# Performance work log

Measured on AMD Instinct MI355X. Metric: run time of the kernel, lower is better.

Reference implementation:

```python
import jax, jax.numpy as jnp
import numpy as np

GRID_SIDES = (16, 32, 64)  # levels=3, base_grid_size=16, expansion=2.0, grid_dimensions=2
BATCH, INPUT_DIM = 8192, 256


def setup_inputs() -> dict:
    key = jax.random.key(0)
    k0, k1, k2, k3 = jax.random.split(key, 4)
    x = jax.random.normal(k0, (BATCH, INPUT_DIM), dtype=jnp.float32)
    w1 = jax.random.normal(k1, (GRID_SIDES[0] ** 2, INPUT_DIM), dtype=jnp.float32)
    w2 = jax.random.normal(k2, (GRID_SIDES[1] ** 2, INPUT_DIM), dtype=jnp.float32)
    w3 = jax.random.normal(k3, (GRID_SIDES[2] ** 2, INPUT_DIM), dtype=jnp.float32)
    return {"x": x, "w1": w1, "w2": w2, "w3": w3}


def _som_level(x, w, side):
    # Squared Euclidean distances (B, N) via the expanded form; N = side*side.
    d2 = (
        jnp.sum(x * x, axis=1, keepdims=True)
        - 2.0 * (x @ w.T)
        + jnp.sum(w * w, axis=1)
    )
    bmu_flat = jnp.argmin(d2, axis=1)  # (B,)
    coords = jnp.stack(jnp.unravel_index(bmu_flat, (side, side)), axis=-1)  # (B, 2)
    # Quantization error = exact Euclidean distance to the BMU prototype.
    diff = x - w[bmu_flat]  # (B, D)
    q_err = jnp.sqrt(jnp.sum(diff * diff, axis=1))  # (B,)
    return coords, q_err


def reference(x, w1, w2, w3):
    c1, q1 = _som_level(x, w1, GRID_SIDES[0])
    c2, q2 = _som_level(x, w2, GRID_SIDES[1])
    c3, q3 = _som_level(x, w3, GRID_SIDES[2])
    return (c1, c2, c3, q1, q2, q3)
```

## Files before the change

### kernel.cpp

```cpp
#include <hip/hip_runtime.h>
#include <hip/hip_fp16.h>
#include <stdint.h>

#define DIM 256
#define KE  768
#define NW  5376

typedef _Float16 half8 __attribute__((ext_vector_type(8)));
typedef float floatx4 __attribute__((ext_vector_type(4)));

#define WS_WE_OFF    12582912
#define WS_WNORM_OFF 20840448
#define WS_XNORM_OFF 20861952
#define WS_BEST_OFF  20894720

__global__ __launch_bounds__(256) void conv_kernel(
    const float* __restrict__ x, const float* __restrict__ w1,
    const float* __restrict__ w2, const float* __restrict__ w3,
    ushort* __restrict__ Xe, ushort* __restrict__ We,
    float* __restrict__ wnorm, float* __restrict__ xnorm,
    unsigned long long* __restrict__ best) {
  if (blockIdx.x < 96) best[blockIdx.x * 256 + threadIdx.x] = ~0ull;
  int task = blockIdx.x * 4 + (threadIdx.x >> 6);
  int lane = threadIdx.x & 63;
  const float* src; ushort* dst; float* ndst; int isx;
  if (task < 8192) {
    src = x + (size_t)task * DIM; dst = Xe + (size_t)task * KE;
    ndst = xnorm + task; isx = 1;
  } else {
    int wi = task - 8192;
    if (wi < 256)       src = w1 + (size_t)wi * DIM;
    else if (wi < 1280) src = w2 + (size_t)(wi - 256) * DIM;
    else                src = w3 + (size_t)(wi - 1280) * DIM;
    dst = We + (size_t)wi * KE; ndst = wnorm + wi; isx = 0;
  }
  float4 v = *(const float4*)(src + lane * 4);
  float fv[4] = {v.x, v.y, v.z, v.w};
  float s = fv[0]*fv[0] + fv[1]*fv[1] + fv[2]*fv[2] + fv[3]*fv[3];
  #pragma unroll
  for (int o = 32; o > 0; o >>= 1) s += __shfl_xor(s, o);
  if (lane == 0) *ndst = s;

  ushort h[4], l[4];
  #pragma unroll
  for (int e = 0; e < 4; ++e) {
    __half hh = __float2half(fv[e]);
    float hf = __half2float(hh);
    __half ll = __float2half((fv[e] - hf) * 2048.0f);
    h[e] = __half_as_ushort(hh);
    l[e] = __half_as_ushort(ll);
  }
  ushort4 h4 = make_ushort4(h[0], h[1], h[2], h[3]);
  ushort4 l4 = make_ushort4(l[0], l[1], l[2], l[3]);
  if (isx) {
    *(ushort4*)(dst + lane * 4)        = h4;
    *(ushort4*)(dst + 256 + lane * 4)  = h4;
    *(ushort4*)(dst + 512 + lane * 4)  = l4;
  } else {
    *(ushort4*)(dst + lane * 4)        = h4;
    *(ushort4*)(dst + 256 + lane * 4)  = l4;
    *(ushort4*)(dst + 512 + lane * 4)  = h4;
  }
}

__global__ __launch_bounds__(256) void gemm_kernel(
    const ushort* __restrict__ Xe, const ushort* __restrict__ We,
    const float* __restrict__ xnorm, const float* __restrict__ wnorm,
    unsigned long long* __restrict__ best) {
  __shared__ __align__(16) ushort As[128 * 64];
  __shared__ __align__(16) ushort Bs[128 * 64];
  unsigned long long (*red)[128] = (unsigned long long (*)[128])As;

  const int cb = blockIdx.x;
  const int r0 = blockIdx.y * 128;
  const int n0 = cb * 128;
  int level, lbase;
  if (cb < 2)       { level = 0; lbase = 0; }
  else if (cb < 10) { level = 1; lbase = 256; }
  else              { level = 2; lbase = 1280; }

  const int t = threadIdx.x;
  const int w = t >> 6;
  const int lane = t & 63;
  const int ln = lane & 15, q = lane >> 4;
  const int wm = (w >> 1) * 64, wn = (w & 1) * 64;

  floatx4 acc[4][4];
  #pragma unroll
  for (int i = 0; i < 4; ++i)
    #pragma unroll
    for (int j = 0; j < 4; ++j) acc[i][j] = (floatx4)0.0f;

  for (int k0 = 0; k0 < KE; k0 += 64) {
    if (k0 == 256) {
      #pragma unroll
      for (int i = 0; i < 4; ++i)
        #pragma unroll
        for (int j = 0; j < 4; ++j) acc[i][j] *= 2048.0f;
    }
    #pragma unroll
    for (int it = 0; it < 4; ++it) {
      int p = it * 256 + t;
      int m = p >> 3;
      int c = (p & 7) ^ (m & 7);
      const ushort* ga = Xe + (size_t)(r0 + m) * KE + k0 + c * 8;
      const ushort* gb = We + (size_t)(n0 + m) * KE + k0 + c * 8;
      int lbase_chunks = it * 256 + (t & 192);
      __builtin_amdgcn_global_load_lds(
          (const __attribute__((address_space(1))) void*)ga,
          (__attribute__((address_space(3))) void*)(As + lbase_chunks * 8), 16, 0, 0);
      __builtin_amdgcn_global_load_lds(
          (const __attribute__((address_space(1))) void*)gb,
          (__attribute__((address_space(3))) void*)(Bs + lbase_chunks * 8), 16, 0, 0);
    }
    __syncthreads();
    #pragma unroll
    for (int s = 0; s < 2; ++s) {
      half8 a[4], b[4];
      #pragma unroll
      for (int mt = 0; mt < 4; ++mt) {
        int m = wm + mt * 16 + ln;
        int pos = m * 8 + ((s * 4 + q) ^ (m & 7));
        a[mt] = *(const half8*)&As[pos * 8];
      }
      #pragma unroll
      for (int nt = 0; nt < 4; ++nt) {
        int n = wn + nt * 16 + ln;
        int pos = n * 8 + ((s * 4 + q) ^ (n & 7));
        b[nt] = *(const half8*)&Bs[pos * 8];
      }
      #pragma unroll
      for (int mt = 0; mt < 4; ++mt)
        #pragma unroll
        for (int nt = 0; nt < 4; ++nt)
          acc[mt][nt] = __builtin_amdgcn_mfma_f32_16x16x32_f16(
              a[mt], b[nt], acc[mt][nt], 0, 0, 0);
    }
    __syncthreads();
  }

  float wnv[4];
  #pragma unroll
  for (int nt = 0; nt < 4; ++nt) wnv[nt] = wnorm[n0 + wn + nt * 16 + ln];

  #pragma unroll
  for (int mt = 0; mt < 4; ++mt) {
    #pragma unroll
    for (int r = 0; r < 4; ++r) {
      int rowl = wm + mt * 16 + q * 4 + r;
      float xnv = xnorm[r0 + rowl];
      unsigned long long bp = ~0ull;
      #pragma unroll
      for (int nt = 0; nt < 4; ++nt) {
        float d2 = fmaxf(xnv + wnv[nt] - acc[mt][nt][r] * 0.0009765625f, 0.0f);
        unsigned col = (unsigned)(n0 + wn + nt * 16 + ln - lbase);
        unsigned long long p =
            ((unsigned long long)__float_as_uint(d2) << 32) | col;
        bp = (p < bp) ? p : bp;
      }
      #pragma unroll
      for (int off = 1; off < 16; off <<= 1) {
        unsigned long long o = __shfl_xor(bp, off);
        bp = (o < bp) ? o : bp;
      }
      if (ln == 0) red[w & 1][rowl] = bp;
    }
  }
  __syncthreads();
  if (t < 128) {
    unsigned long long a = red[0][t], b = red[1][t];
    unsigned long long m = (a < b) ? a : b;
    atomicMin(&best[level * 8192 + r0 + t], m);
  }
}

__global__ __launch_bounds__(256) void finalize_kernel(
    const float* __restrict__ x, const float* __restrict__ w1,
    const float* __restrict__ w2, const float* __restrict__ w3,
    const unsigned long long* __restrict__ best, float* __restrict__ out) {
  int task = blockIdx.x * 4 + (threadIdx.x >> 6);
  int lane = threadIdx.x & 63;
  int level = task >> 13;
  int row = task & 8191;
  const float* w; unsigned side;
  if (level == 0)      { w = w1; side = 16; }
  else if (level == 1) { w = w2; side = 32; }
  else                 { w = w3; side = 64; }
  unsigned idx = (unsigned)(best[level * 8192 + row] & 0xFFFFFFFFull);
  float4 xv = *(const float4*)(x + (size_t)row * DIM + lane * 4);
  float4 wv = *(const float4*)(w + (size_t)idx * DIM + lane * 4);
  float dx = xv.x - wv.x, dy = xv.y - wv.y, dz = xv.z - wv.z, dw = xv.w - wv.w;
  float s = dx * dx + dy * dy + dz * dz + dw * dw;
  #pragma unroll
  for (int o = 32; o > 0; o >>= 1) s += __shfl_xor(s, o);
  if (lane == 0) {
    out[level * 16384 + row * 2 + 0] = (float)(idx / side);
    out[level * 16384 + row * 2 + 1] = (float)(idx % side);
    out[49152 + level * 8192 + row] = sqrtf(s);
  }
}

extern "C" void kernel_launch(void* const* d_in, const int* in_sizes, int n_in,
                              void* d_out, int out_size, void* d_ws, size_t ws_size,
                              hipStream_t stream) {
  const float* x  = (const float*)d_in[0];
  const float* w1 = (const float*)d_in[1];
  const float* w2 = (const float*)d_in[2];
  const float* w3 = (const float*)d_in[3];
  ushort* Xe = (ushort*)d_ws;
  ushort* We = (ushort*)((char*)d_ws + WS_WE_OFF);
  float* wnorm = (float*)((char*)d_ws + WS_WNORM_OFF);
  float* xnorm = (float*)((char*)d_ws + WS_XNORM_OFF);
  unsigned long long* best = (unsigned long long*)((char*)d_ws + WS_BEST_OFF);

  conv_kernel<<<3392, 256, 0, stream>>>(x, w1, w2, w3, Xe, We, wnorm, xnorm,
                                        best);
  gemm_kernel<<<dim3(42, 64), 256, 0, stream>>>(Xe, We, xnorm, wnorm, best);
  finalize_kernel<<<6144, 256, 0, stream>>>(x, w1, w2, w3, best, (float*)d_out);
}
```

Baseline: 162.8 us.

## Fuse conv, GEMM and finalize into one persistent kernel with grid barriers

Replaces the three kernel launches with a single persistent kernel of 896 blocks. Work items are grid-strided, and the phases are separated by software grid barriers built on an atomic counter that is reset by a memset. The aim is to remove launch gaps and tail effects between the phases. In exchange it adds barrier spin cost and a memset, relies on all blocks being co-resident (launch_bounds 256,5), and caps spinning with a timeout that could let a phase start early.

New measurement: 565.9 us. 248% more time.

```diff
diff --git a/kernel.cpp b/kernel.cpp
--- a/kernel.cpp
+++ b/kernel.cpp
@@ -4,7 +4,7 @@
 
 #define DIM 256
 #define KE  768
-#define NW  5376
+#define NBLK 896
 
 typedef _Float16 half8 __attribute__((ext_vector_type(8)));
 typedef float floatx4 __attribute__((ext_vector_type(4)));
@@ -13,190 +13,207 @@
 #define WS_WNORM_OFF 20840448
 #define WS_XNORM_OFF 20861952
 #define WS_BEST_OFF  20894720
-
-__global__ __launch_bounds__(256) void conv_kernel(
+#define WS_CTRL_OFF  21091328
+
+__device__ __forceinline__ void grid_barrier(unsigned* cnt, unsigned target) {
+  __syncthreads();
+  if (threadIdx.x == 0) {
+    __threadfence();
+    atomicAdd(cnt, 1u);
+    unsigned spins = 0;
+    while (atomicAdd(cnt, 0u) < target && spins < 4000000u) {
+      __builtin_amdgcn_s_sleep(2);
+      ++spins;
+    }
+    __threadfence();
+  }
+  __syncthreads();
+}
+
+__global__ __launch_bounds__(256, 5) void fused_kernel(
     const float* __restrict__ x, const float* __restrict__ w1,
     const float* __restrict__ w2, const float* __restrict__ w3,
     ushort* __restrict__ Xe, ushort* __restrict__ We,
     float* __restrict__ wnorm, float* __restrict__ xnorm,
-    unsigned long long* __restrict__ best) {
-  if (blockIdx.x < 96) best[blockIdx.x * 256 + threadIdx.x] = ~0ull;
-  int task = blockIdx.x * 4 + (threadIdx.x >> 6);
-  int lane = threadIdx.x & 63;
-  const float* src; ushort* dst; float* ndst; int isx;
-  if (task < 8192) {
-    src = x + (size_t)task * DIM; dst = Xe + (size_t)task * KE;
-    ndst = xnorm + task; isx = 1;
-  } else {
-    int wi = task - 8192;
-    if (wi < 256)       src = w1 + (size_t)wi * DIM;
-    else if (wi < 1280) src = w2 + (size_t)(wi - 256) * DIM;
-    else                src = w3 + (size_t)(wi - 1280) * DIM;
-    dst = We + (size_t)wi * KE; ndst = wnorm + wi; isx = 0;
-  }
-  float4 v = *(const float4*)(src + lane * 4);
-  float fv[4] = {v.x, v.y, v.z, v.w};
-  float s = fv[0]*fv[0] + fv[1]*fv[1] + fv[2]*fv[2] + fv[3]*fv[3];
-  #pragma unroll
-  for (int o = 32; o > 0; o >>= 1) s += __shfl_xor(s, o);
-  if (lane == 0) *ndst = s;
-
-  ushort h[4], l[4];
-  #pragma unroll
-  for (int e = 0; e < 4; ++e) {
-    __half hh = __float2half(fv[e]);
-    float hf = __half2float(hh);
-    __half ll = __float2half((fv[e] - hf) * 2048.0f);
-    h[e] = __half_as_ushort(hh);
-    l[e] = __half_as_ushort(ll);
-  }
-  ushort4 h4 = make_ushort4(h[0], h[1], h[2], h[3]);
-  ushort4 l4 = make_ushort4(l[0], l[1], l[2], l[3]);
-  if (isx) {
-    *(ushort4*)(dst + lane * 4)        = h4;
-    *(ushort4*)(dst + 256 + lane * 4)  = h4;
-    *(ushort4*)(dst + 512 + lane * 4)  = l4;
-  } else {
-    *(ushort4*)(dst + lane * 4)        = h4;
-    *(ushort4*)(dst + 256 + lane * 4)  = l4;
-    *(ushort4*)(dst + 512 + lane * 4)  = h4;
-  }
-}
-
-__global__ __launch_bounds__(256) void gemm_kernel(
-    const ushort* __restrict__ Xe, const ushort* __restrict__ We,
-    const float* __restrict__ xnorm, const float* __restrict__ wnorm,
-    unsigned long long* __restrict__ best) {
+    unsigned long long* __restrict__ best, unsigned* __restrict__ ctrl,
+    float* __restrict__ out) {
   __shared__ __align__(16) ushort As[128 * 64];
   __shared__ __align__(16) ushort Bs[128 * 64];
   unsigned long long (*red)[128] = (unsigned long long (*)[128])As;
 
-  const int cb = blockIdx.x;
-  const int r0 = blockIdx.y * 128;
-  const int n0 = cb * 128;
-  int level, lbase;
-  if (cb < 2)       { level = 0; lbase = 0; }
-  else if (cb < 10) { level = 1; lbase = 256; }
-  else              { level = 2; lbase = 1280; }
-
   const int t = threadIdx.x;
-  const int w = t >> 6;
+  const int wv = t >> 6;
   const int lane = t & 63;
+
+  if (blockIdx.x < 96) best[blockIdx.x * 256 + t] = ~0ull;
+  for (int task = blockIdx.x * 4 + wv; task < 13568; task += NBLK * 4) {
+    const float* src; ushort* dst; float* ndst; int isx;
+    if (task < 8192) {
+      src = x + (size_t)task * DIM; dst = Xe + (size_t)task * KE;
+      ndst = xnorm + task; isx = 1;
+    } else {
+      int wi = task - 8192;
+      if (wi < 256)       src = w1 + (size_t)wi * DIM;
+      else if (wi < 1280) src = w2 + (size_t)(wi - 256) * DIM;
+      else                src = w3 + (size_t)(wi - 1280) * DIM;
+      dst = We + (size_t)wi * KE; ndst = wnorm + wi; isx = 0;
+    }
+    float4 v = *(const float4*)(src + lane * 4);
+    float fv[4] = {v.x, v.y, v.z, v.w};
+    float s = fv[0]*fv[0] + fv[1]*fv[1] + fv[2]*fv[2] + fv[3]*fv[3];
+    #pragma unroll
+    for (int o = 32; o > 0; o >>= 1) s += __shfl_xor(s, o);
+    if (lane == 0) *ndst = s;
+
+    ushort h[4], l[4];
+    #pragma unroll
+    for (int e = 0; e < 4; ++e) {
+      __half hh = __float2half(fv[e]);
+      float hf = __half2float(hh);
+      __half ll = __float2half((fv[e] - hf) * 2048.0f);
+      h[e] = __half_as_ushort(hh);
+      l[e] = __half_as_ushort(ll);
+    }
+    ushort4 h4 = make_ushort4(h[0], h[1], h[2], h[3]);
+    ushort4 l4 = make_ushort4(l[0], l[1], l[2], l[3]);
+    if (isx) {
+      *(ushort4*)(dst + lane * 4)        = h4;
+      *(ushort4*)(dst + 256 + lane * 4)  = h4;
+      *(ushort4*)(dst + 512 + lane * 4)  = l4;
+    } else {
+      *(ushort4*)(dst + lane * 4)        = h4;
+      *(ushort4*)(dst + 256 + lane * 4)  = l4;
+      *(ushort4*)(dst + 512 + lane * 4)  = h4;
+    }
+  }
+  grid_barrier(ctrl, NBLK);
+
   const int ln = lane & 15, q = lane >> 4;
-  const int wm = (w >> 1) * 64, wn = (w & 1) * 64;
-
-  floatx4 acc[4][4];
-  #pragma unroll
-  for (int i = 0; i < 4; ++i)
-    #pragma unroll
-    for (int j = 0; j < 4; ++j) acc[i][j] = (floatx4)0.0f;
-
-  for (int k0 = 0; k0 < KE; k0 += 64) {
-    if (k0 == 256) {
-      #pragma unroll
-      for (int i = 0; i < 4; ++i)
-        #pragma unroll
-        for (int j = 0; j < 4; ++j) acc[i][j] *= 2048.0f;
-    }
-    #pragma unroll
-    for (int it = 0; it < 4; ++it) {
-      int p = it * 256 + t;
-      int m = p >> 3;
-      int c = (p & 7) ^ (m & 7);
-      const ushort* ga = Xe + (size_t)(r0 + m) * KE + k0 + c * 8;
-      const ushort* gb = We + (size_t)(n0 + m) * KE + k0 + c * 8;
-      int lbase_chunks = it * 256 + (t & 192);
-      __builtin_amdgcn_global_load_lds(
-          (const __attribute__((address_space(1))) void*)ga,
-          (__attribute__((address_space(3))) void*)(As + lbase_chunks * 8), 16, 0, 0);
-      __builtin_amdgcn_global_load_lds(
-          (const __attribute__((address_space(1))) void*)gb,
-          (__attribute__((address_space(3))) void*)(Bs + lbase_chunks * 8), 16, 0, 0);
-    }
+  const int wm = (wv >> 1) * 64, wn = (wv & 1) * 64;
+
+  for (int tb = blockIdx.x; tb < 2688; tb += NBLK) {
+    const int cb = tb % 42;
+    const int r0 = (tb / 42) * 128;
+    const int n0 = cb * 128;
+    int level, lbase;
+    if (cb < 2)       { level = 0; lbase = 0; }
+    else if (cb < 10) { level = 1; lbase = 256; }
+    else              { level = 2; lbase = 1280; }
+
     __syncthreads();
-    #pragma unroll
-    for (int s = 0; s < 2; ++s) {
-      half8 a[4], b[4];
-      #pragma unroll
-      for (int mt = 0; mt < 4; ++mt) {
-        int m = wm + mt * 16 + ln;
-        int pos = m * 8 + ((s * 4 + q) ^ (m & 7));
-        a[mt] = *(const half8*)&As[pos * 8];
-      }
-      #pragma unroll
-      for (int nt = 0; nt < 4; ++nt) {
-        int n = wn + nt * 16 + ln;
-        int pos = n * 8 + ((s * 4 + q) ^ (n & 7));
-        b[nt] = *(const half8*)&Bs[pos * 8];
-      }
-      #pragma unroll
-      for (int mt = 0; mt < 4; ++mt)
-        #pragma unroll
-        for (int nt = 0; nt < 4; ++nt)
-          acc[mt][nt] = __builtin_amdgcn_mfma_f32_16x16x32_f16(
-              a[mt], b[nt], acc[mt][nt], 0, 0, 0);
+
+    floatx4 acc[4][4];
+    #pragma unroll
+    for (int i = 0; i < 4; ++i)
+      #pragma unroll
+      for (int j = 0; j < 4; ++j) acc[i][j] = (floatx4)0.0f;
+
+    for (int k0 = 0; k0 < KE; k0 += 64) {
+      if (k0 == 256) {
+        #pragma unroll
+        for (int i = 0; i < 4; ++i)
+          #pragma unroll
+          for (int j = 0; j < 4; ++j) acc[i][j] *= 2048.0f;
+      }
+      #pragma unroll
+      for (int it = 0; it < 4; ++it) {
+        int p = it * 256 + t;
+        int m = p >> 3;
+        int c = (p & 7) ^ (m & 7);
+        const ushort* ga = Xe + (size_t)(r0 + m) * KE + k0 + c * 8;
+        const ushort* gb = We + (size_t)(n0 + m) * KE + k0 + c * 8;
+        int lbc = it * 256 + (t & 192);
+        __builtin_amdgcn_global_load_lds(
+            (const __attribute__((address_space(1))) void*)ga,
+            (__attribute__((address_space(3))) void*)(As + lbc * 8), 16, 0, 0);
+        __builtin_amdgcn_global_load_lds(
+            (const __attribute__((address_space(1))) void*)gb,
+            (__attribute__((address_space(3))) void*)(Bs + lbc * 8), 16, 0, 0);
+      }
+      __syncthreads();
+      #pragma unroll
+      for (int s = 0; s < 2; ++s) {
+        half8 a[4], b[4];
+        #pragma unroll
+        for (int mt = 0; mt < 4; ++mt) {
+          int m = wm + mt * 16 + ln;
+          int pos = m * 8 + ((s * 4 + q) ^ (m & 7));
+          a[mt] = *(const half8*)&As[pos * 8];
+        }
+        #pragma unroll
+        for (int nt = 0; nt < 4; ++nt) {
+          int n = wn + nt * 16 + ln;
+          int pos = n * 8 + ((s * 4 + q) ^ (n & 7));
+          b[nt] = *(const half8*)&Bs[pos * 8];
+        }
+        #pragma unroll
+        for (int mt = 0; mt < 4; ++mt)
+          #pragma unroll
+          for (int nt = 0; nt < 4; ++nt)
+            acc[mt][nt] = __builtin_amdgcn_mfma_f32_16x16x32_f16(
+                a[mt], b[nt], acc[mt][nt], 0, 0, 0);
+      }
+      __syncthreads();
+    }
+
+    float wnv[4];
+    #pragma unroll
+    for (int nt = 0; nt < 4; ++nt) wnv[nt] = wnorm[n0 + wn + nt * 16 + ln];
+
+    #pragma unroll
+    for (int mt = 0; mt < 4; ++mt) {
+      #pragma unroll
+      for (int r = 0; r < 4; ++r) {
+        int rowl = wm + mt * 16 + q * 4 + r;
+        float xnv = xnorm[r0 + rowl];
+        unsigned long long bp = ~0ull;
+        #pragma unroll
+        for (int nt = 0; nt < 4; ++nt) {
+          float d2 = fmaxf(xnv + wnv[nt] - acc[mt][nt][r] * 0.0009765625f,
+                           0.0f);
+          unsigned col = (unsigned)(n0 + wn + nt * 16 + ln - lbase);
+          unsigned long long p =
+              ((unsigned long long)__float_as_uint(d2) << 32) | col;
+          bp = (p < bp) ? p : bp;
+        }
+        #pragma unroll
+        for (int off = 1; off < 16; off <<= 1) {
+          unsigned long long o = __shfl_xor(bp, off);
+          bp = (o < bp) ? o : bp;
+        }
+        if (ln == 0) red[wv & 1][rowl] = bp;
+      }
     }
     __syncthreads();
-  }
-
-  float wnv[4];
-  #pragma unroll
-  for (int nt = 0; nt < 4; ++nt) wnv[nt] = wnorm[n0 + wn + nt * 16 + ln];
-
-  #pragma unroll
-  for (int mt = 0; mt < 4; ++mt) {
-    #pragma unroll
-    for (int r = 0; r < 4; ++r) {
-      int rowl = wm + mt * 16 + q * 4 + r;
-      float xnv = xnorm[r0 + rowl];
-      unsigned long long bp = ~0ull;
-      #pragma unroll
-      for (int nt = 0; nt < 4; ++nt) {
-        float d2 = fmaxf(xnv + wnv[nt] - acc[mt][nt][r] * 0.0009765625f, 0.0f);
-        unsigned col = (unsigned)(n0 + wn + nt * 16 + ln - lbase);
-        unsigned long long p =
-            ((unsigned long long)__float_as_uint(d2) << 32) | col;
-        bp = (p < bp) ? p : bp;
-      }
-      #pragma unroll
-      for (int off = 1; off < 16; off <<= 1) {
-        unsigned long long o = __shfl_xor(bp, off);
-        bp = (o < bp) ? o : bp;
-      }
-      if (ln == 0) red[w & 1][rowl] = bp;
-    }
-  }
-  __syncthreads();
-  if (t < 128) {
-    unsigned long long a = red[0][t], b = red[1][t];
-    unsigned long long m = (a < b) ? a : b;
-    atomicMin(&best[level * 8192 + r0 + t], m);
-  }
-}
-
-__global__ __launch_bounds__(256) void finalize_kernel(
-    const float* __restrict__ x, const float* __restrict__ w1,
-    const float* __restrict__ w2, const float* __restrict__ w3,
-    const unsigned long long* __restrict__ best, float* __restrict__ out) {
-  int task = blockIdx.x * 4 + (threadIdx.x >> 6);
-  int lane = threadIdx.x & 63;
-  int level = task >> 13;
-  int row = task & 8191;
-  const float* w; unsigned side;
-  if (level == 0)      { w = w1; side = 16; }
-  else if (level == 1) { w = w2; side = 32; }
-  else                 { w = w3; side = 64; }
-  unsigned idx = (unsigned)(best[level * 8192 + row] & 0xFFFFFFFFull);
-  float4 xv = *(const float4*)(x + (size_t)row * DIM + lane * 4);
-  float4 wv = *(const float4*)(w + (size_t)idx * DIM + lane * 4);
-  float dx = xv.x - wv.x, dy = xv.y - wv.y, dz = xv.z - wv.z, dw = xv.w - wv.w;
-  float s = dx * dx + dy * dy + dz * dz + dw * dw;
-  #pragma unroll
-  for (int o = 32; o > 0; o >>= 1) s += __shfl_xor(s, o);
-  if (lane == 0) {
-    out[level * 16384 + row * 2 + 0] = (float)(idx / side);
-    out[level * 16384 + row * 2 + 1] = (float)(idx % side);
-    out[49152 + level * 8192 + row] = sqrtf(s);
+    if (t < 128) {
+      unsigned long long a = red[0][t], b = red[1][t];
+      unsigned long long m = (a < b) ? a : b;
+      atomicMin(&best[level * 8192 + r0 + t], m);
+    }
+  }
+  grid_barrier(ctrl, 2 * NBLK);
+
+  for (int task = blockIdx.x * 4 + wv; task < 24576; task += NBLK * 4) {
+    int level = task >> 13;
+    int row = task & 8191;
+    const float* w; unsigned side;
+    if (level == 0)      { w = w1; side = 16; }
+    else if (level == 1) { w = w2; side = 32; }
+    else                 { w = w3; side = 64; }
+    unsigned idx = (unsigned)(best[task] & 0xFFFFFFFFull);
+    if (idx >= side * side) idx = 0;
+    float4 xv = *(const float4*)(x + (size_t)row * DIM + lane * 4);
+    float4 wvv = *(const float4*)(w + (size_t)idx * DIM + lane * 4);
+    float dx = xv.x - wvv.x, dy = xv.y - wvv.y;
+    float dz = xv.z - wvv.z, dw = xv.w - wvv.w;
+    float s = dx * dx + dy * dy + dz * dz + dw * dw;
+    #pragma unroll
+    for (int o = 32; o > 0; o >>= 1) s += __shfl_xor(s, o);
+    if (lane == 0) {
+      out[level * 16384 + row * 2 + 0] = (float)(idx / side);
+      out[level * 16384 + row * 2 + 1] = (float)(idx % side);
+      out[49152 + level * 8192 + row] = sqrtf(s);
+    }
   }
 }
 
@@ -212,9 +229,9 @@
   float* wnorm = (float*)((char*)d_ws + WS_WNORM_OFF);
   float* xnorm = (float*)((char*)d_ws + WS_XNORM_OFF);
   unsigned long long* best = (unsigned long long*)((char*)d_ws + WS_BEST_OFF);
-
-  conv_kernel<<<3392, 256, 0, stream>>>(x, w1, w2, w3, Xe, We, wnorm, xnorm,
-                                        best);
-  gemm_kernel<<<dim3(42, 64), 256, 0, stream>>>(Xe, We, xnorm, wnorm, best);
-  finalize_kernel<<<6144, 256, 0, stream>>>(x, w1, w2, w3, best, (float*)d_out);
+  unsigned* ctrl = (unsigned*)((char*)d_ws + WS_CTRL_OFF);
+
+  hipMemsetAsync(ctrl, 0, 64, stream);
+  fused_kernel<<<NBLK, 256, 0, stream>>>(x, w1, w2, w3, Xe, We, wnorm, xnorm,
+                                         best, ctrl, (float*)d_out);
 }
```

## Store split-fp16 operands once and reuse the GEMM min distance for quantization error

Applied to the files above, without the earlier changes.

The conversion kernel now writes only the hi and lo fp16 halves (512 elements per row instead of three 256-element segments). The GEMM remaps its K offsets so the three split-product passes read the right halves from the smaller buffers, which cuts workspace traffic. The finalize kernel no longer gathers x and the BMU prototype to recompute the exact distance. It takes the sqrt of the expanded-form d2 already packed into the atomicMin key and clamps out-of-range indices. This drops a full pass over x and the weights, at the cost of a quantization error from the expanded formula that may differ slightly from the exact direct difference.

Measured after the change: 163.2 us. About the same (+0.3%).

```diff
diff --git a/kernel.cpp b/kernel.cpp
--- a/kernel.cpp
+++ b/kernel.cpp
@@ -4,15 +4,14 @@
 
 #define DIM 256
 #define KE  768
-#define NW  5376
 
 typedef _Float16 half8 __attribute__((ext_vector_type(8)));
 typedef float floatx4 __attribute__((ext_vector_type(4)));
 
-#define WS_WE_OFF    12582912
-#define WS_WNORM_OFF 20840448
-#define WS_XNORM_OFF 20861952
-#define WS_BEST_OFF  20894720
+#define WS_WE_OFF    8388608
+#define WS_WNORM_OFF 13893632
+#define WS_XNORM_OFF 13915136
+#define WS_BEST_OFF  13947904
 
 __global__ __launch_bounds__(256) void conv_kernel(
     const float* __restrict__ x, const float* __restrict__ w1,
@@ -23,16 +22,16 @@
   if (blockIdx.x < 96) best[blockIdx.x * 256 + threadIdx.x] = ~0ull;
   int task = blockIdx.x * 4 + (threadIdx.x >> 6);
   int lane = threadIdx.x & 63;
-  const float* src; ushort* dst; float* ndst; int isx;
+  const float* src; ushort* dst; float* ndst;
   if (task < 8192) {
-    src = x + (size_t)task * DIM; dst = Xe + (size_t)task * KE;
-    ndst = xnorm + task; isx = 1;
+    src = x + (size_t)task * DIM; dst = Xe + (size_t)task * 512;
+    ndst = xnorm + task;
   } else {
     int wi = task - 8192;
     if (wi < 256)       src = w1 + (size_t)wi * DIM;
     else if (wi < 1280) src = w2 + (size_t)(wi - 256) * DIM;
     else                src = w3 + (size_t)(wi - 1280) * DIM;
-    dst = We + (size_t)wi * KE; ndst = wnorm + wi; isx = 0;
+    dst = We + (size_t)wi * 512; ndst = wnorm + wi;
   }
   float4 v = *(const float4*)(src + lane * 4);
   float fv[4] = {v.x, v.y, v.z, v.w};
@@ -50,17 +49,8 @@
     h[e] = __half_as_ushort(hh);
     l[e] = __half_as_ushort(ll);
   }
-  ushort4 h4 = make_ushort4(h[0], h[1], h[2], h[3]);
-  ushort4 l4 = make_ushort4(l[0], l[1], l[2], l[3]);
-  if (isx) {
-    *(ushort4*)(dst + lane * 4)        = h4;
-    *(ushort4*)(dst + 256 + lane * 4)  = h4;
-    *(ushort4*)(dst + 512 + lane * 4)  = l4;
-  } else {
-    *(ushort4*)(dst + lane * 4)        = h4;
-    *(ushort4*)(dst + 256 + lane * 4)  = l4;
-    *(ushort4*)(dst + 512 + lane * 4)  = h4;
-  }
+  *(ushort4*)(dst + lane * 4)       = make_ushort4(h[0], h[1], h[2], h[3]);
+  *(ushort4*)(dst + 256 + lane * 4) = make_ushort4(l[0], l[1], l[2], l[3]);
 }
 
 __global__ __launch_bounds__(256) void gemm_kernel(
@@ -98,20 +88,22 @@
         #pragma unroll
         for (int j = 0; j < 4; ++j) acc[i][j] *= 2048.0f;
     }
+    const int ak0 = (k0 < 512) ? (k0 & 255) : (k0 - 256);
+    const int bk0 = (k0 < 512) ? k0 : (k0 - 512);
     #pragma unroll
     for (int it = 0; it < 4; ++it) {
       int p = it * 256 + t;
       int m = p >> 3;
       int c = (p & 7) ^ (m & 7);
-      const ushort* ga = Xe + (size_t)(r0 + m) * KE + k0 + c * 8;
-      const ushort* gb = We + (size_t)(n0 + m) * KE + k0 + c * 8;
-      int lbase_chunks = it * 256 + (t & 192);
+      const ushort* ga = Xe + (size_t)(r0 + m) * 512 + ak0 + c * 8;
+      const ushort* gb = We + (size_t)(n0 + m) * 512 + bk0 + c * 8;
+      int lbc = it * 256 + (t & 192);
       __builtin_amdgcn_global_load_lds(
           (const __attribute__((address_space(1))) void*)ga,
-          (__attribute__((address_space(3))) void*)(As + lbase_chunks * 8), 16, 0, 0);
+          (__attribute__((address_space(3))) void*)(As + lbc * 8), 16, 0, 0);
       __builtin_amdgcn_global_load_lds(
           (const __attribute__((address_space(1))) void*)gb,
-          (__attribute__((address_space(3))) void*)(Bs + lbase_chunks * 8), 16, 0, 0);
+          (__attribute__((address_space(3))) void*)(Bs + lbc * 8), 16, 0, 0);
     }
     __syncthreads();
     #pragma unroll
@@ -175,29 +167,18 @@
 }
 
 __global__ __launch_bounds__(256) void finalize_kernel(
-    const float* __restrict__ x, const float* __restrict__ w1,
-    const float* __restrict__ w2, const float* __restrict__ w3,
     const unsigned long long* __restrict__ best, float* __restrict__ out) {
-  int task = blockIdx.x * 4 + (threadIdx.x >> 6);
-  int lane = threadIdx.x & 63;
+  int task = blockIdx.x * 256 + threadIdx.x;
   int level = task >> 13;
   int row = task & 8191;
-  const float* w; unsigned side;
-  if (level == 0)      { w = w1; side = 16; }
-  else if (level == 1) { w = w2; side = 32; }
-  else                 { w = w3; side = 64; }
-  unsigned idx = (unsigned)(best[level * 8192 + row] & 0xFFFFFFFFull);
-  float4 xv = *(const float4*)(x + (size_t)row * DIM + lane * 4);
-  float4 wv = *(const float4*)(w + (size_t)idx * DIM + lane * 4);
-  float dx = xv.x - wv.x, dy = xv.y - wv.y, dz = xv.z - wv.z, dw = xv.w - wv.w;
-  float s = dx * dx + dy * dy + dz * dz + dw * dw;
-  #pragma unroll
-  for (int o = 32; o > 0; o >>= 1) s += __shfl_xor(s, o);
-  if (lane == 0) {
-    out[level * 16384 + row * 2 + 0] = (float)(idx / side);
-    out[level * 16384 + row * 2 + 1] = (float)(idx % side);
-    out[49152 + level * 8192 + row] = sqrtf(s);
-  }
+  unsigned side = (level == 0) ? 16u : (level == 1) ? 32u : 64u;
+  unsigned long long v = best[task];
+  unsigned idx = (unsigned)(v & 0xFFFFFFFFull);
+  if (idx >= side * side) idx = 0;
+  float d2 = __uint_as_float((unsigned)(v >> 32));
+  out[level * 16384 + row * 2 + 0] = (float)(idx / side);
+  out[level * 16384 + row * 2 + 1] = (float)(idx % side);
+  out[49152 + level * 8192 + row] = sqrtf(d2);
 }
 
 extern "C" void kernel_launch(void* const* d_in, const int* in_sizes, int n_in,
@@ -216,5 +197,5 @@
   conv_kernel<<<3392, 256, 0, stream>>>(x, w1, w2, w3, Xe, We, wnorm, xnorm,
                                         best);
   gemm_kernel<<<dim3(42, 64), 256, 0, stream>>>(Xe, We, xnorm, wnorm, best);
-  finalize_kernel<<<6144, 256, 0, stream>>>(x, w1, w2, w3, best, (float*)d_out);
-}
+  finalize_kernel<<<96, 256, 0, stream>>>(best, (float*)d_out);
+}
```
